# Kernel optimization log

Measured on AMD Instinct MI355X. Metric: run time of the kernel, lower is better.

## Reference

```python
import jax, jax.numpy as jnp
import numpy as np

GAMMA = 0.99
GAE_LAMBDA = 0.95
DONE_PROB = 0.01  # sparse episode terminations, typical for long-horizon trading envs


def setup_inputs() -> dict:
    key = jax.random.key(0)
    k1, k2, k3 = jax.random.split(key, 3)
    T, N = 2048, 4096  # rollout_len, num_envs
    rewards = jax.random.normal(k1, (T, N), dtype=jnp.float32)
    values = jax.random.normal(k2, (T, N), dtype=jnp.float32)
    dones = (jax.random.uniform(k3, (T, N)) < DONE_PROB).astype(jnp.float32)
    return {"rewards": rewards, "values": values, "dones": dones}


def reference(rewards, values, dones):
    # rewards/values/dones: [T, N]
    T, N = rewards.shape
    # bootstrap: beyond the last step, next_value = 0 and next_done = 1
    next_value = jnp.concatenate([values[1:], jnp.zeros((1, N), values.dtype)], axis=0)
    next_done = jnp.concatenate([dones[1:], jnp.ones((1, N), dones.dtype)], axis=0)
    nonterminal = 1.0 - next_done                      # [T, N]
    delta = rewards + GAMMA * next_value * nonterminal - values  # [T, N]

    def step(last_adv, xs):
        d, nt = xs                                     # each [N]
        adv = d + GAMMA * GAE_LAMBDA * nt * last_adv
        return adv, adv

    init = jnp.zeros((N,), rewards.dtype)
    _, advantages = jax.lax.scan(step, init, (delta, nonterminal), reverse=True)
    returns = advantages + values
    return advantages, returns
```

## Files before the change

### kernel.cpp

```cpp
#include <hip/hip_runtime.h>


#define T_LEN    2048
#define N_ENV    4096
#define N_CHUNKS 64
#define CHUNK_L  (T_LEN / N_CHUNKS)

__constant__ float kGamma_unused;

static constexpr float GAMMA = 0.99f;
static constexpr float GL    = 0.99f * 0.95f;

__global__ __launch_bounds__(256) void gae_phase1(
    const float* __restrict__ rewards,
    const float* __restrict__ values,
    const float* __restrict__ dones,
    float* __restrict__ Aout,
    float* __restrict__ Pout)
{
    const int idx = blockIdx.x * blockDim.x + threadIdx.x;
    if (idx >= N_CHUNKS * N_ENV) return;
    const int n = idx & (N_ENV - 1);
    const int c = idx >> 12;
    const int t_hi = c * CHUNK_L + (CHUNK_L - 1);

    float v_next, d_next;
    if (c == N_CHUNKS - 1) { v_next = 0.0f; d_next = 1.0f; }
    else {
        v_next = values[(t_hi + 1) * N_ENV + n];
        d_next = dones [(t_hi + 1) * N_ENV + n];
    }

    const float* rp = rewards + (size_t)t_hi * N_ENV + n;
    const float* vp = values  + (size_t)t_hi * N_ENV + n;
    const float* dp = dones   + (size_t)t_hi * N_ENV + n;

    float A = 1.0f, P = 0.0f;
    #pragma unroll 4
    for (int i = 0; i < CHUNK_L; ++i) {
        const float r = *rp, v = *vp, d = *dp;
        const float nt    = 1.0f - d_next;
        const float delta = fmaf(GAMMA * v_next, nt, r) - v;
        const float cc    = GL * nt;
        P = fmaf(cc, P, delta);
        A = cc * A;
        v_next = v; d_next = d;
        rp -= N_ENV; vp -= N_ENV; dp -= N_ENV;
    }
    Aout[idx] = A;
    Pout[idx] = P;
}

__global__ __launch_bounds__(256) void gae_phase2(
    const float* __restrict__ Ain,
    const float* __restrict__ Pin,
    float* __restrict__ inc)
{
    const int n = blockIdx.x * blockDim.x + threadIdx.x;
    if (n >= N_ENV) return;
    float b = 0.0f;
    for (int c = N_CHUNKS - 1; c >= 0; --c) {
        inc[c * N_ENV + n] = b;
        b = fmaf(Ain[c * N_ENV + n], b, Pin[c * N_ENV + n]);
    }
}

__global__ __launch_bounds__(256) void gae_phase3(
    const float* __restrict__ rewards,
    const float* __restrict__ values,
    const float* __restrict__ dones,
    const float* __restrict__ inc,
    float* __restrict__ out)
{
    const int idx = blockIdx.x * blockDim.x + threadIdx.x;
    if (idx >= N_CHUNKS * N_ENV) return;
    const int n = idx & (N_ENV - 1);
    const int c = idx >> 12;
    const int t_hi = c * CHUNK_L + (CHUNK_L - 1);

    float v_next, d_next;
    if (c == N_CHUNKS - 1) { v_next = 0.0f; d_next = 1.0f; }
    else {
        v_next = values[(t_hi + 1) * N_ENV + n];
        d_next = dones [(t_hi + 1) * N_ENV + n];
    }

    const float* rp = rewards + (size_t)t_hi * N_ENV + n;
    const float* vp = values  + (size_t)t_hi * N_ENV + n;
    const float* dp = dones   + (size_t)t_hi * N_ENV + n;
    float*       ap = out     + (size_t)t_hi * N_ENV + n;
    float*       gp = out     + (size_t)(T_LEN + t_hi) * N_ENV + n;

    float adv = inc[idx];
    #pragma unroll 4
    for (int i = 0; i < CHUNK_L; ++i) {
        const float r = *rp, v = *vp, d = *dp;
        const float nt    = 1.0f - d_next;
        const float delta = fmaf(GAMMA * v_next, nt, r) - v;
        const float cc    = GL * nt;
        adv = fmaf(cc, adv, delta);
        *ap = adv;
        *gp = adv + v;
        v_next = v; d_next = d;
        rp -= N_ENV; vp -= N_ENV; dp -= N_ENV;
        ap -= N_ENV; gp -= N_ENV;
    }
}

extern "C" void kernel_launch(void* const* d_in, const int* in_sizes, int n_in,
                              void* d_out, int out_size, void* d_ws, size_t ws_size,
                              hipStream_t stream) {
    const float* rewards = (const float*)d_in[0];
    const float* values  = (const float*)d_in[1];
    const float* dones   = (const float*)d_in[2];
    float* out = (float*)d_out;

    float* A   = (float*)d_ws;
    float* P   = A + (size_t)N_CHUNKS * N_ENV;
    float* inc = P + (size_t)N_CHUNKS * N_ENV;

    const int total = N_CHUNKS * N_ENV;
    const int blk = 256;

    gae_phase1<<<total / blk, blk, 0, stream>>>(rewards, values, dones, A, P);
    gae_phase2<<<N_ENV / blk, blk, 0, stream>>>(A, P, inc);
    gae_phase3<<<total / blk, blk, 0, stream>>>(rewards, values, dones, inc, out);
}
```

Measured before the change: 177.8 us.

## Vectorize scan phases with float4 and parallelize chunk carry via wave shuffle scan

Result: faster. 169.9 us (-4.5%).

```diff
diff --git a/kernel.cpp b/kernel.cpp
--- a/kernel.cpp
+++ b/kernel.cpp
@@ -3,49 +3,53 @@
 
 #define T_LEN    2048
 #define N_ENV    4096
+#define NV4      (N_ENV / 4)
 #define N_CHUNKS 64
 #define CHUNK_L  (T_LEN / N_CHUNKS)
-
-__constant__ float kGamma_unused;
 
 static constexpr float GAMMA = 0.99f;
 static constexpr float GL    = 0.99f * 0.95f;
 
 __global__ __launch_bounds__(256) void gae_phase1(
-    const float* __restrict__ rewards,
-    const float* __restrict__ values,
-    const float* __restrict__ dones,
-    float* __restrict__ Aout,
-    float* __restrict__ Pout)
+    const float4* __restrict__ rewards,
+    const float4* __restrict__ values,
+    const float4* __restrict__ dones,
+    float4* __restrict__ Aout,
+    float4* __restrict__ Pout)
 {
     const int idx = blockIdx.x * blockDim.x + threadIdx.x;
-    if (idx >= N_CHUNKS * N_ENV) return;
-    const int n = idx & (N_ENV - 1);
-    const int c = idx >> 12;
+    if (idx >= N_CHUNKS * NV4) return;
+    const int n4 = idx & (NV4 - 1);
+    const int c  = idx >> 10;
     const int t_hi = c * CHUNK_L + (CHUNK_L - 1);
 
-    float v_next, d_next;
-    if (c == N_CHUNKS - 1) { v_next = 0.0f; d_next = 1.0f; }
-    else {
-        v_next = values[(t_hi + 1) * N_ENV + n];
-        d_next = dones [(t_hi + 1) * N_ENV + n];
+    float4 v_next, d_next;
+    if (c == N_CHUNKS - 1) {
+        v_next = make_float4(0.f, 0.f, 0.f, 0.f);
+        d_next = make_float4(1.f, 1.f, 1.f, 1.f);
+    } else {
+        v_next = values[(t_hi + 1) * NV4 + n4];
+        d_next = dones [(t_hi + 1) * NV4 + n4];
     }
 
-    const float* rp = rewards + (size_t)t_hi * N_ENV + n;
-    const float* vp = values  + (size_t)t_hi * N_ENV + n;
-    const float* dp = dones   + (size_t)t_hi * N_ENV + n;
+    float4 A = make_float4(1.f, 1.f, 1.f, 1.f);
+    float4 P = make_float4(0.f, 0.f, 0.f, 0.f);
 
-    float A = 1.0f, P = 0.0f;
-    #pragma unroll 4
+    #pragma unroll 8
     for (int i = 0; i < CHUNK_L; ++i) {
-        const float r = *rp, v = *vp, d = *dp;
-        const float nt    = 1.0f - d_next;
-        const float delta = fmaf(GAMMA * v_next, nt, r) - v;
-        const float cc    = GL * nt;
-        P = fmaf(cc, P, delta);
-        A = cc * A;
-        v_next = v; d_next = d;
-        rp -= N_ENV; vp -= N_ENV; dp -= N_ENV;
+        const int t = t_hi - i;
+        const float4 r = rewards[t * NV4 + n4];
+        const float4 v = values [t * NV4 + n4];
+        const float4 d = dones  [t * NV4 + n4];
+        #define STEP(X) { \
+            const float nt    = 1.0f - d_next.X; \
+            const float delta = fmaf(GAMMA * v_next.X, nt, r.X) - v.X; \
+            const float cc    = GL * nt; \
+            P.X = fmaf(cc, P.X, delta); \
+            A.X = cc * A.X; \
+            v_next.X = v.X; d_next.X = d.X; }
+        STEP(x) STEP(y) STEP(z) STEP(w)
+        #undef STEP
     }
     Aout[idx] = A;
     Pout[idx] = P;
@@ -56,73 +60,88 @@
     const float* __restrict__ Pin,
     float* __restrict__ inc)
 {
-    const int n = blockIdx.x * blockDim.x + threadIdx.x;
+    const int tid  = blockIdx.x * blockDim.x + threadIdx.x;
+    const int n    = tid >> 6;
+    const int lane = tid & 63;
     if (n >= N_ENV) return;
-    float b = 0.0f;
-    for (int c = N_CHUNKS - 1; c >= 0; --c) {
-        inc[c * N_ENV + n] = b;
-        b = fmaf(Ain[c * N_ENV + n], b, Pin[c * N_ENV + n]);
+
+    float Ax = Ain[lane * N_ENV + n];
+    float Px = Pin[lane * N_ENV + n];
+
+    #pragma unroll
+    for (int off = 1; off < 64; off <<= 1) {
+        const float Ap = __shfl_down(Ax, off, 64);
+        const float Pp = __shfl_down(Px, off, 64);
+        const bool valid = (lane + off) < 64;
+        const float Pn = valid ? fmaf(Ax, Pp, Px) : Px;
+        const float An = valid ? Ax * Ap       : Ax;
+        Px = Pn; Ax = An;
     }
+    const float bP = __shfl_down(Px, 1, 64);
+    inc[lane * N_ENV + n] = (lane == 63) ? 0.0f : bP;
 }
 
 __global__ __launch_bounds__(256) void gae_phase3(
-    const float* __restrict__ rewards,
-    const float* __restrict__ values,
-    const float* __restrict__ dones,
-    const float* __restrict__ inc,
-    float* __restrict__ out)
+    const float4* __restrict__ rewards,
+    const float4* __restrict__ values,
+    const float4* __restrict__ dones,
+    const float4* __restrict__ inc,
+    float4* __restrict__ out)
 {
     const int idx = blockIdx.x * blockDim.x + threadIdx.x;
-    if (idx >= N_CHUNKS * N_ENV) return;
-    const int n = idx & (N_ENV - 1);
-    const int c = idx >> 12;
+    if (idx >= N_CHUNKS * NV4) return;
+    const int n4 = idx & (NV4 - 1);
+    const int c  = idx >> 10;
     const int t_hi = c * CHUNK_L + (CHUNK_L - 1);
 
-    float v_next, d_next;
-    if (c == N_CHUNKS - 1) { v_next = 0.0f; d_next = 1.0f; }
-    else {
-        v_next = values[(t_hi + 1) * N_ENV + n];
-        d_next = dones [(t_hi + 1) * N_ENV + n];
+    float4 v_next, d_next;
+    if (c == N_CHUNKS - 1) {
+        v_next = make_float4(0.f, 0.f, 0.f, 0.f);
+        d_next = make_float4(1.f, 1.f, 1.f, 1.f);
+    } else {
+        v_next = values[(t_hi + 1) * NV4 + n4];
+        d_next = dones [(t_hi + 1) * NV4 + n4];
     }
 
-    const float* rp = rewards + (size_t)t_hi * N_ENV + n;
-    const float* vp = values  + (size_t)t_hi * N_ENV + n;
-    const float* dp = dones   + (size_t)t_hi * N_ENV + n;
-    float*       ap = out     + (size_t)t_hi * N_ENV + n;
-    float*       gp = out     + (size_t)(T_LEN + t_hi) * N_ENV + n;
+    float4 adv = inc[idx];
 
-    float adv = inc[idx];
-    #pragma unroll 4
+    #pragma unroll 8
     for (int i = 0; i < CHUNK_L; ++i) {
-        const float r = *rp, v = *vp, d = *dp;
-        const float nt    = 1.0f - d_next;
-        const float delta = fmaf(GAMMA * v_next, nt, r) - v;
-        const float cc    = GL * nt;
-        adv = fmaf(cc, adv, delta);
-        *ap = adv;
-        *gp = adv + v;
-        v_next = v; d_next = d;
-        rp -= N_ENV; vp -= N_ENV; dp -= N_ENV;
-        ap -= N_ENV; gp -= N_ENV;
+        const int t = t_hi - i;
+        const float4 r = rewards[t * NV4 + n4];
+        const float4 v = values [t * NV4 + n4];
+        const float4 d = dones  [t * NV4 + n4];
+        float4 ret;
+        #define STEP(X) { \
+            const float nt    = 1.0f - d_next.X; \
+            const float delta = fmaf(GAMMA * v_next.X, nt, r.X) - v.X; \
+            const float cc    = GL * nt; \
+            adv.X = fmaf(cc, adv.X, delta); \
+            ret.X = adv.X + v.X; \
+            v_next.X = v.X; d_next.X = d.X; }
+        STEP(x) STEP(y) STEP(z) STEP(w)
+        #undef STEP
+        out[t * NV4 + n4]           = adv;
+        out[(T_LEN + t) * NV4 + n4] = ret;
     }
 }
 
 extern "C" void kernel_launch(void* const* d_in, const int* in_sizes, int n_in,
                               void* d_out, int out_size, void* d_ws, size_t ws_size,
                               hipStream_t stream) {
-    const float* rewards = (const float*)d_in[0];
-    const float* values  = (const float*)d_in[1];
-    const float* dones   = (const float*)d_in[2];
-    float* out = (float*)d_out;
+    const float4* rewards = (const float4*)d_in[0];
+    const float4* values  = (const float4*)d_in[1];
+    const float4* dones   = (const float4*)d_in[2];
+    float4* out = (float4*)d_out;
 
     float* A   = (float*)d_ws;
     float* P   = A + (size_t)N_CHUNKS * N_ENV;
     float* inc = P + (size_t)N_CHUNKS * N_ENV;
 
-    const int total = N_CHUNKS * N_ENV;
     const int blk = 256;
-
-    gae_phase1<<<total / blk, blk, 0, stream>>>(rewards, values, dones, A, P);
-    gae_phase2<<<N_ENV / blk, blk, 0, stream>>>(A, P, inc);
-    gae_phase3<<<total / blk, blk, 0, stream>>>(rewards, values, dones, inc, out);
+    gae_phase1<<<(N_CHUNKS * NV4) / blk, blk, 0, stream>>>(
+        rewards, values, dones, (float4*)A, (float4*)P);
+    gae_phase2<<<(N_ENV * 64) / blk, blk, 0, stream>>>(A, P, inc);
+    gae_phase3<<<(N_CHUNKS * NV4) / blk, blk, 0, stream>>>(
+        rewards, values, dones, (const float4*)inc, out);
 }
```
